# Performance work log

Hardware: AMD Instinct MI355X
Metric: run time of the kernel (lower is better)

Reference implementation:

```python
import jax, jax.numpy as jnp
import numpy as np

DIM = 1024
NUM_HEADS = 16
NUM_GROUPS = 4
HEAD_DIM = DIM // NUM_HEADS          # 64
HPG = NUM_HEADS // NUM_GROUPS        # heads per group = 4
SCALE = 1.0 / np.sqrt(HEAD_DIM)
LN_EPS = 1e-5


def layer_norm(x, w, b):
    # LayerNorm over last dim (head_dim), biased variance like torch.
    m = jnp.mean(x, axis=-1, keepdims=True)
    v = jnp.mean(jnp.square(x - m), axis=-1, keepdims=True)
    return (x - m) * jax.lax.rsqrt(v + LN_EPS) * w + b


def setup_inputs() -> dict:
    key = jax.random.key(0)
    ks = jax.random.split(key, 16)
    B, Q, KV = 2, 2048, 2048
    inv = 1.0 / np.sqrt(DIM)
    return {
        "query": jax.random.normal(ks[0], (B, Q, DIM), jnp.float32),
        "key": jax.random.normal(ks[1], (B, KV, DIM), jnp.float32),
        "value": jax.random.normal(ks[2], (B, KV, DIM), jnp.float32),
        "attn_mask": jnp.ones((B, Q, KV), dtype=bool),
        "Wq": jax.random.normal(ks[3], (DIM, DIM), jnp.float32) * inv,
        "bq": jnp.zeros((DIM,), jnp.float32),
        "Wk": jax.random.normal(ks[4], (NUM_GROUPS * HEAD_DIM, DIM), jnp.float32) * inv,
        "bk": jnp.zeros((NUM_GROUPS * HEAD_DIM,), jnp.float32),
        "Wv": jax.random.normal(ks[5], (NUM_GROUPS * HEAD_DIM, DIM), jnp.float32) * inv,
        "bv": jnp.zeros((NUM_GROUPS * HEAD_DIM,), jnp.float32),
        "q_norm_w": jnp.ones((HEAD_DIM,), jnp.float32),
        "q_norm_b": jnp.zeros((HEAD_DIM,), jnp.float32),
        "k_norm_w": jnp.ones((HEAD_DIM,), jnp.float32),
        "k_norm_b": jnp.zeros((HEAD_DIM,), jnp.float32),
        "Wo": jax.random.normal(ks[6], (DIM, DIM), jnp.float32) * inv,
        "bo": jnp.zeros((DIM,), jnp.float32),
    }


def reference(query, key, value, attn_mask, Wq, bq, Wk, bk, Wv, bv,
              q_norm_w, q_norm_b, k_norm_w, k_norm_b, Wo, bo):
    B, Q, _ = query.shape
    KV = key.shape[1]
    # projections (torch nn.Linear: x @ W.T + b)
    q = query @ Wq.T + bq                     # [B,Q,dim]
    k = key @ Wk.T + bk                       # [B,KV,G*hd]
    v = value @ Wv.T + bv                     # [B,KV,G*hd]
    # split heads: q -> [B, G, hpg, Q, hd]
    q = q.reshape(B, Q, NUM_GROUPS, HPG, HEAD_DIM).transpose(0, 2, 3, 1, 4)
    # k, v -> [B, G, KV, hd], broadcast over hpg
    k = k.reshape(B, KV, NUM_GROUPS, HEAD_DIM).transpose(0, 2, 1, 3)
    v = v.reshape(B, KV, NUM_GROUPS, HEAD_DIM).transpose(0, 2, 1, 3)
    # QK-norm per head_dim
    q = layer_norm(q, q_norm_w, q_norm_b)     # [B,G,hpg,Q,hd]
    k = layer_norm(k, k_norm_w, k_norm_b)     # [B,G,KV,hd]
    # attention scores: [B,G,hpg,Q,KV]
    scores = jnp.einsum('bghqd,bgkd->bghqk', q, k) * SCALE
    neg = jnp.asarray(jnp.finfo(scores.dtype).min, scores.dtype)
    scores = jnp.where(attn_mask[:, None, None, :, :], scores, neg)
    attn = jax.nn.softmax(scores, axis=-1)
    out = jnp.einsum('bghqk,bgkd->bghqd', attn, v)   # [B,G,hpg,Q,hd]
    out = out.transpose(0, 3, 1, 2, 4).reshape(B, Q, DIM)
    return out @ Wo.T + bo
```

## Files before the change

kernel.cpp:

```cpp
#include <hip/hip_runtime.h>
#include <math.h>

#define DIM   1024
#define NH    16
#define NG    4
#define HD    64
#define SEQ   2048
#define NB    2
#define SCALE 0.125f
#define LN_EPS 1e-5f
#define LOG2E 1.44269504f
#define QS    (SCALE * LOG2E)

#if __has_builtin(__builtin_amdgcn_exp2f)
#define EXP2F(x) __builtin_amdgcn_exp2f(x)
#else
#define EXP2F(x) __expf((x) * 0.69314718f)
#endif

typedef __attribute__((ext_vector_type(8)))  short short8;
typedef __attribute__((ext_vector_type(4)))  short short4v;
typedef __attribute__((ext_vector_type(4)))  float f32x4;
typedef __attribute__((ext_vector_type(16))) float f32x16;
typedef __attribute__((ext_vector_type(4)))  uint  uint4v;
typedef unsigned short ushort;
typedef unsigned int uint;

__device__ __forceinline__ ushort f2b(float f) {
  uint u = __builtin_bit_cast(uint, f);
  u += 0x7FFFu + ((u >> 16) & 1u);
  return (ushort)(u >> 16);
}
__device__ __forceinline__ uint pack2(float a, float b) {
  return (uint)f2b(a) | ((uint)f2b(b) << 16);
}
__device__ __forceinline__ uint packtr(float a, float b) {
  return __builtin_amdgcn_perm(__builtin_bit_cast(uint, b),
                               __builtin_bit_cast(uint, a), 0x07060302u);
}
__device__ __forceinline__ void gload16(const void* g, void* l) {
  __builtin_amdgcn_global_load_lds(
      (const __attribute__((address_space(1))) void*)g,
      (__attribute__((address_space(3))) void*)l, 16, 0, 0);
}

struct CastSeg { const float* s; ushort* d; int nblk; };
struct CastArgs { CastSeg seg[7]; };

__global__ __launch_bounds__(256) void castN(CastArgs a) {
  for (int t0 = blockIdx.x; t0 < 7424; t0 += gridDim.x) {
    int t = t0, i = 0;
    while (i < 6 && t >= a.seg[i].nblk) { t -= a.seg[i].nblk; ++i; }
    const float* src = a.seg[i].s;
    ushort* dst = a.seg[i].d;
    size_t idx = (size_t)t * 2048 + threadIdx.x * 8;
    float4 f0 = *(const float4*)(src + idx);
    float4 f1 = *(const float4*)(src + idx + 4);
    short8 o;
    o[0] = (short)f2b(f0.x); o[1] = (short)f2b(f0.y);
    o[2] = (short)f2b(f0.z); o[3] = (short)f2b(f0.w);
    o[4] = (short)f2b(f1.x); o[5] = (short)f2b(f1.y);
    o[6] = (short)f2b(f1.z); o[7] = (short)f2b(f1.w);
    *(short8*)(dst + idx) = o;
  }
}

#define STAGE2(dstLDS, srcG, NROWS, kk)                                        \
  _Pragma("unroll")                                                            \
  for (int i = 0; i < (NROWS) / 32; ++i) {                                     \
    int s = i * 256 + tid;                                                     \
    int row = s >> 3, cg = (s & 7) ^ (row & 7);                                \
    gload16(&(srcG)[(size_t)row * DIM + (kk) + cg * 8],                        \
            &(dstLDS)[(size_t)(i * 256 + (wave << 6)) * 8]);                   \
  }

#define CORE_128x64(Aptr, Wbase)                                               \
  f32x4 acc[2][4] = {};                                                        \
  { const int wm0 = wave * 32;                                                 \
    const ushort* Arows = (Aptr) + (size_t)m0 * DIM;                           \
    STAGE2(As[0], Arows, 128, 0)                                               \
    STAGE2(Ws[0], (Wbase), 64, 0)                                              \
    _Pragma("unroll")                                                          \
    for (int k0 = 0; k0 < DIM; k0 += 64) {                                     \
      const int pb = (k0 >> 6) & 1;                                            \
      __syncthreads();                                                         \
      if (k0 + 64 < DIM) {                                                     \
        STAGE2(As[1 - pb], Arows, 128, k0 + 64)                                \
        STAGE2(Ws[1 - pb], (Wbase), 64, k0 + 64)                               \
      }                                                                        \
      _Pragma("unroll")                                                        \
      for (int kh = 0; kh < 2; ++kh) {                                         \
        short8 af[2], bfr[4];                                                  \
        _Pragma("unroll")                                                      \
        for (int mt = 0; mt < 2; ++mt) {                                       \
          int row = wm0 + mt * 16 + l16;                                       \
          int st = (kh * 4 + quad) ^ (row & 7);                                \
          af[mt] = *(const short8*)&As[pb][row * 64 + st * 8];                 \
        }                                                                      \
        _Pragma("unroll")                                                      \
        for (int nt = 0; nt < 4; ++nt) {                                       \
          int row = nt * 16 + l16;                                             \
          int st = (kh * 4 + quad) ^ (row & 7);                                \
          bfr[nt] = *(const short8*)&Ws[pb][row * 64 + st * 8];                \
        }                                                                      \
        _Pragma("unroll")                                                      \
        for (int mt = 0; mt < 2; ++mt)                                         \
          _Pragma("unroll")                                                    \
          for (int nt = 0; nt < 4; ++nt)                                       \
            acc[mt][nt] = __builtin_amdgcn_mfma_f32_16x16x32_bf16(             \
                af[mt], bfr[nt], acc[mt][nt], 0, 0, 0);                        \
      }                                                                        \
    } }

#define LN_EPI(MT, rowbase, biasp, lnwp, lnbp, psv, outp, ostride, colb)       \
  { float bw[4], lw[4], lb[4];                                                 \
    _Pragma("unroll") for (int nt = 0; nt < 4; ++nt) {                         \
      bw[nt] = biasp[(colb) + nt * 16 + l16];                                  \
      lw[nt] = lnwp[nt * 16 + l16];                                            \
      lb[nt] = lnbp[nt * 16 + l16]; }                                          \
    _Pragma("unroll") for (int mt = 0; mt < (MT); ++mt) {                      \
      _Pragma("unroll") for (int r = 0; r < 4; ++r) {                          \
        float x0 = acc[mt][0][r] + bw[0];                                      \
        float x1 = acc[mt][1][r] + bw[1];                                      \
        float x2 = acc[mt][2][r] + bw[2];                                      \
        float x3 = acc[mt][3][r] + bw[3];                                      \
        float s1 = x0 + x1 + x2 + x3;                                          \
        float s2 = x0 * x0 + x1 * x1 + x2 * x2 + x3 * x3;                      \
        _Pragma("unroll") for (int off = 1; off < 16; off <<= 1) {             \
          s1 += __shfl_xor(s1, off, 64); s2 += __shfl_xor(s2, off, 64); }      \
        float mean = s1 * (1.f / 64.f);                                        \
        float var  = s2 * (1.f / 64.f) - mean * mean;                          \
        float inv  = rsqrtf(var + LN_EPS);                                     \
        int row = (rowbase) + mt * 16 + quad * 4 + r;                          \
        ushort* dst = outp + (size_t)row * (ostride) + (colb) + l16;           \
        dst[ 0] = f2b(((x0 - mean) * inv * lw[0] + lb[0]) * (psv));            \
        dst[16] = f2b(((x1 - mean) * inv * lw[1] + lb[1]) * (psv));            \
        dst[32] = f2b(((x2 - mean) * inv * lw[2] + lb[2]) * (psv));            \
        dst[48] = f2b(((x3 - mean) * inv * lw[3] + lb[3]) * (psv)); } } }

__global__ __launch_bounds__(256) void gemm_qkv(
    const ushort* __restrict__ qA, const ushort* __restrict__ kA,
    const ushort* __restrict__ vA,
    const ushort* __restrict__ WqB, const ushort* __restrict__ WkB,
    const ushort* __restrict__ WvB,
    const float* __restrict__ bq, const float* __restrict__ bk,
    const float* __restrict__ bv,
    const float* __restrict__ qnw, const float* __restrict__ qnb,
    const float* __restrict__ knw, const float* __restrict__ knb,
    ushort* __restrict__ Qb, ushort* __restrict__ kbb, ushort* __restrict__ vtb)
{
  __shared__ __align__(16) ushort As[2][128 * 64];
  __shared__ __align__(16) ushort Ws[2][64 * 64];
  const int bid = blockIdx.x;
  const int sw = (bid & 7) * 96 + (bid >> 3);
  const int x = sw % 24;
  const int tid = threadIdx.x;
  const int wave = tid >> 6, lane = tid & 63;
  const int quad = lane >> 4, l16 = lane & 15;
  const int m0 = (sw / 24) * 128;

  if (x < 16) {
    const ushort* Wbase = WqB + (size_t)x * 64 * DIM;
    CORE_128x64(qA, Wbase)
    LN_EPI(2, m0 + wave * 32, bq, qnw, qnb, QS, Qb, DIM, x * 64)
  } else if (x < 20) {
    const int n0 = (x - 16) * 64;
    const ushort* Wbase = WkB + (size_t)n0 * DIM;
    CORE_128x64(kA, Wbase)
    LN_EPI(2, m0 + wave * 32, bk, knw, knb, 1.0f, kbb, NG * HD, n0)
  } else {
    const int g = x - 20;
    const ushort* Wbase = WvB + (size_t)g * 64 * DIM;
    CORE_128x64(vA, Wbase)
#pragma unroll
    for (int nt = 0; nt < 4; ++nt) {
      int d = nt * 16 + l16;
      float bvv = bv[g * 64 + d];
#pragma unroll
      for (int mt = 0; mt < 2; ++mt)
#pragma unroll
        for (int r = 0; r < 4; ++r) {
          int row = m0 + wave * 32 + mt * 16 + quad * 4 + r;
          int bb = row >> 11, kv = row & (SEQ - 1);
          int kvp = (kv & ~12) | ((kv & 4) << 1) | ((kv & 8) >> 1);
          vtb[((size_t)(bb * NG + g) * HD + d) * SEQ + kvp] =
              f2b(acc[mt][nt][r] + bvv);
        }
    }
  }
}

__global__ __launch_bounds__(256) void gemm_out(
    const ushort* __restrict__ A, const ushort* __restrict__ WoB,
    const float* __restrict__ bo, float* __restrict__ Cf)
{
  __shared__ __align__(16) ushort As[2][128 * 64];
  __shared__ __align__(16) ushort Ws[2][64 * 64];
  const int bid = blockIdx.x;
  const int sw = (bid & 7) * 64 + (bid >> 3);
  const int tid = threadIdx.x;
  const int wave = tid >> 6, lane = tid & 63;
  const int quad = lane >> 4, l16 = lane & 15;
  const int m0 = (sw >> 4) * 128;
  const int n0 = (sw & 15) * 64;
  const ushort* Wbase = WoB + (size_t)n0 * DIM;
  CORE_128x64(A, Wbase)
#pragma unroll
  for (int nt = 0; nt < 4; ++nt) {
    int col = n0 + nt * 16 + l16;
    float bvv = bo[col];
#pragma unroll
    for (int mt = 0; mt < 2; ++mt)
#pragma unroll
      for (int r = 0; r < 4; ++r) {
        int row = m0 + wave * 32 + mt * 16 + quad * 4 + r;
        Cf[(size_t)row * DIM + col] = acc[mt][nt][r] + bvv;
      }
  }
}

__global__ __launch_bounds__(256) void attn_mfma4(
    const ushort* __restrict__ qb,
    const ushort* __restrict__ kb,
    const ushort* __restrict__ vt,
    ushort* __restrict__ op)
{
  __shared__ __align__(16) ushort SM[2][16384];
  const int bid = blockIdx.x;
  const int xcd = bid & 7, rest = bid >> 3;
  const int b = xcd >> 2, g = xcd & 3;
  const int h = g * 4 + (rest & 3);
  const int qt = rest >> 2;
  const int tid = threadIdx.x;
  const int wave = tid >> 6, lane = tid & 63;
  const int l32 = lane & 31, hf = lane >> 5;
  const int q0 = qt << 7;

  short8 qf[4];
  {
    const ushort* qp = qb + (size_t)(b * SEQ + q0 + wave * 32 + l32) * DIM
                          + h * HD + hf * 8;
#pragma unroll
    for (int ks = 0; ks < 4; ++ks) qf[ks] = *(const short8*)(qp + ks * 16);
  }

#define STAGE_ATTN(PB, KV0)                                                    \
  _Pragma("unroll")                                                            \
  for (int i = 0; i < 4; ++i) {                                                \
    int s = i * 256 + tid;                                                     \
    int rowK = s >> 3, cgK = (s & 7) ^ (rowK & 7);                             \
    gload16(&kb[(size_t)(b * SEQ + (KV0) + rowK) * (NG * HD) + g * HD + cgK * 8],\
            &SM[PB][(size_t)(i * 256 + (wave << 6)) * 8]);                     \
    int rowV = s >> 4, cgV = (s & 15) ^ (rowV & 7);                            \
    gload16(&vt[((size_t)(b * NG + g) * HD + rowV) * SEQ + (KV0) + cgV * 8],   \
            &SM[PB][8192 + (size_t)(i * 256 + (wave << 6)) * 8]);              \
  }

  f32x16 O0 = {0,0,0,0,0,0,0,0,0,0,0,0,0,0,0,0};
  f32x16 O1 = {0,0,0,0,0,0,0,0,0,0,0,0,0,0,0,0};
  float lsum = 0.f;

  STAGE_ATTN(0, 0)
  __syncthreads();

  for (int kv0 = 0; kv0 < SEQ; kv0 += 128) {
    const int pb = (kv0 >> 7) & 1;
    if (kv0 + 128 < SEQ) { STAGE_ATTN(1 - pb, kv0 + 128) }
    const ushort* Ks = SM[pb];
    const ushort* Vs = SM[pb] + 8192;

    f32x16 S0 = {0,0,0,0,0,0,0,0,0,0,0,0,0,0,0,0};
    f32x16 S1 = {0,0,0,0,0,0,0,0,0,0,0,0,0,0,0,0};
    f32x16 S2 = {0,0,0,0,0,0,0,0,0,0,0,0,0,0,0,0};
    f32x16 S3 = {0,0,0,0,0,0,0,0,0,0,0,0,0,0,0,0};
    __builtin_amdgcn_s_setprio(1);
#pragma unroll
    for (int ks = 0; ks < 4; ++ks) {
      short8 k0 = *(const short8*)&Ks[( 0 + l32) * 64 + (((ks*2+hf) ^ ( l32 & 7)) * 8)];
      short8 k1 = *(const short8*)&Ks[(32 + l32) * 64 + (((ks*2+hf) ^ ( l32 & 7)) * 8)];
      short8 k2 = *(const short8*)&Ks[(64 + l32) * 64 + (((ks*2+hf) ^ ( l32 & 7)) * 8)];
      short8 k3 = *(const short8*)&Ks[(96 + l32) * 64 + (((ks*2+hf) ^ ( l32 & 7)) * 8)];
      S0 = __builtin_amdgcn_mfma_f32_32x32x16_bf16(k0, qf[ks], S0, 0, 0, 0);
      S1 = __builtin_amdgcn_mfma_f32_32x32x16_bf16(k1, qf[ks], S1, 0, 0, 0);
      S2 = __builtin_amdgcn_mfma_f32_32x32x16_bf16(k2, qf[ks], S2, 0, 0, 0);
      S3 = __builtin_amdgcn_mfma_f32_32x32x16_bf16(k3, qf[ks], S3, 0, 0, 0);
    }
    __builtin_amdgcn_s_setprio(0);

#pragma unroll
    for (int t = 0; t < 8; ++t) {
      const f32x16& Ss = (t < 2) ? S0 : (t < 4) ? S1 : (t < 6) ? S2 : S3;
      int base = (t & 1) * 8;
      float e0 = EXP2F(Ss[base + 0]), e1 = EXP2F(Ss[base + 1]);
      float e2 = EXP2F(Ss[base + 2]), e3 = EXP2F(Ss[base + 3]);
      float e4 = EXP2F(Ss[base + 4]), e5 = EXP2F(Ss[base + 5]);
      float e6 = EXP2F(Ss[base + 6]), e7 = EXP2F(Ss[base + 7]);
      lsum += ((e0 + e1) + (e2 + e3)) + ((e4 + e5) + (e6 + e7));
      uint4v pw;
      pw[0] = packtr(e0, e1); pw[1] = packtr(e2, e3);
      pw[2] = packtr(e4, e5); pw[3] = packtr(e6, e7);
      short8 pf = __builtin_bit_cast(short8, pw);
      int ch = (t * 2 + hf);
      short8 v0 = *(const short8*)&Vs[( 0 + l32) * 128 + ((ch ^ ( l32 & 7)) * 8)];
      short8 v1 = *(const short8*)&Vs[(32 + l32) * 128 + ((ch ^ ( l32 & 7)) * 8)];
      __builtin_amdgcn_s_setprio(1);
      O0 = __builtin_amdgcn_mfma_f32_32x32x16_bf16(v0, pf, O0, 0, 0, 0);
      O1 = __builtin_amdgcn_mfma_f32_32x32x16_bf16(v1, pf, O1, 0, 0, 0);
      __builtin_amdgcn_s_setprio(0);
    }
    __syncthreads();
  }

  float inv = 1.f / (lsum + __shfl_xor(lsum, 32, 64));

  ushort* Lw = (ushort*)SM + wave * (32 * 68);
#pragma unroll
  for (int r = 0; r < 16; r += 2) {
    int d0 = (r & 3) + 8 * (r >> 2) + 4 * hf;
    *(uint*)&Lw[l32 * 68 + d0]      = pack2(O0[r] * inv, O0[r + 1] * inv);
    *(uint*)&Lw[l32 * 68 + 32 + d0] = pack2(O1[r] * inv, O1[r + 1] * inv);
  }
  ushort* orow = op + (size_t)(b * SEQ + q0 + wave * 32 + l32) * DIM
                    + h * HD + hf * 32;
#pragma unroll
  for (int c = 0; c < 4; ++c) {
    short4v lo = *(const short4v*)&Lw[l32 * 68 + hf * 32 + c * 8];
    short4v hi = *(const short4v*)&Lw[l32 * 68 + hf * 32 + c * 8 + 4];
    short8 o = {lo[0], lo[1], lo[2], lo[3], hi[0], hi[1], hi[2], hi[3]};
    *(short8*)(orow + c * 8) = o;
  }
#undef STAGE_ATTN
}

extern "C" void kernel_launch(void* const* d_in, const int* in_sizes, int n_in,
                              void* d_out, int out_size, void* d_ws, size_t ws_size,
                              hipStream_t stream) {
  (void)in_sizes; (void)n_in; (void)out_size; (void)ws_size;
  const float* query = (const float*)d_in[0];
  const float* key   = (const float*)d_in[1];
  const float* value = (const float*)d_in[2];
  const float* Wq = (const float*)d_in[4];
  const float* bq = (const float*)d_in[5];
  const float* Wk = (const float*)d_in[6];
  const float* bk = (const float*)d_in[7];
  const float* Wv = (const float*)d_in[8];
  const float* bv = (const float*)d_in[9];
  const float* qnw = (const float*)d_in[10];
  const float* qnb = (const float*)d_in[11];
  const float* knw = (const float*)d_in[12];
  const float* knb = (const float*)d_in[13];
  const float* Wo = (const float*)d_in[14];
  const float* bo = (const float*)d_in[15];
  float* out = (float*)d_out;

  const size_t MD = (size_t)NB * SEQ * DIM;
  const size_t WD = (size_t)DIM * DIM;
  const size_t KD = (size_t)(NG * HD) * DIM;
  const size_t MK = (size_t)NB * SEQ * NG * HD;

  ushort* qA  = (ushort*)d_ws;
  ushort* kA  = qA  + MD;
  ushort* WqB = kA  + MD;
  ushort* WkB = WqB + WD;
  ushort* WvB = WkB + KD;
  ushort* WoB = WvB + KD;
  ushort* Qb  = WoB + WD;
  ushort* vA  = (ushort*)d_out;
  ushort* kbb = vA  + MD;
  ushort* vtb = kbb + MK;
  ushort* attnO = kA;

  dim3 blk(256);
  CastArgs ca;
  ca.seg[0] = { query, qA, 2048 };
  ca.seg[1] = { key,   kA, 2048 };
  ca.seg[2] = { value, vA, 2048 };
  ca.seg[3] = { Wq, WqB, 512 };
  ca.seg[4] = { Wk, WkB, 128 };
  ca.seg[5] = { Wv, WvB, 128 };
  ca.seg[6] = { Wo, WoB, 512 };
  castN<<<dim3(1856), blk, 0, stream>>>(ca);
  gemm_qkv<<<dim3(768), blk, 0, stream>>>(
      qA, kA, vA, WqB, WkB, WvB, bq, bk, bv,
      qnw, qnb, knw, knb, Qb, kbb, vtb);
  attn_mfma4<<<dim3(512), blk, 0, stream>>>(Qb, kbb, vtb, attnO);
  gemm_out<<<dim3(512), blk, 0, stream>>>(attnO, WoB, bo, out);
}
```

Baseline: 223.7 us.

## Fuse cast into QKV GEMM and out-proj into attention via grid barriers

Merges the fp32-to-bf16 cast kernel into the QKV projection kernel, and the output projection into the attention kernel, with a software grid-wide atomic barrier between phases. This cuts launches from four to two (plus two small memsets) and removes inter-kernel gaps. The barriers rely on all 768 or 512 blocks being co-resident, which launch_bounds hints encourage but do not guarantee; otherwise the kernel deadlocks. Barrier counters are placed in scratch regions of d_out and the workspace that are reset by memset each call.

Measured after the change: 518.5 us. 132% more time.

```diff
diff --git a/kernel.cpp b/kernel.cpp
--- a/kernel.cpp
+++ b/kernel.cpp
@@ -44,26 +44,21 @@
       (__attribute__((address_space(3))) void*)l, 16, 0, 0);
 }
 
+__device__ __forceinline__ void grid_sync(uint* bar, uint nblk) {
+  __threadfence();
+  __syncthreads();
+  if (threadIdx.x == 0) {
+    __hip_atomic_fetch_add(bar, 1u, __ATOMIC_ACQ_REL, __HIP_MEMORY_SCOPE_AGENT);
+    while (__hip_atomic_load(bar, __ATOMIC_ACQUIRE, __HIP_MEMORY_SCOPE_AGENT)
+           < nblk)
+      __builtin_amdgcn_s_sleep(2);
+  }
+  __syncthreads();
+  __threadfence();
+}
+
 struct CastSeg { const float* s; ushort* d; int nblk; };
 struct CastArgs { CastSeg seg[7]; };
-
-__global__ __launch_bounds__(256) void castN(CastArgs a) {
-  for (int t0 = blockIdx.x; t0 < 7424; t0 += gridDim.x) {
-    int t = t0, i = 0;
-    while (i < 6 && t >= a.seg[i].nblk) { t -= a.seg[i].nblk; ++i; }
-    const float* src = a.seg[i].s;
-    ushort* dst = a.seg[i].d;
-    size_t idx = (size_t)t * 2048 + threadIdx.x * 8;
-    float4 f0 = *(const float4*)(src + idx);
-    float4 f1 = *(const float4*)(src + idx + 4);
-    short8 o;
-    o[0] = (short)f2b(f0.x); o[1] = (short)f2b(f0.y);
-    o[2] = (short)f2b(f0.z); o[3] = (short)f2b(f0.w);
-    o[4] = (short)f2b(f1.x); o[5] = (short)f2b(f1.y);
-    o[6] = (short)f2b(f1.z); o[7] = (short)f2b(f1.w);
-    *(short8*)(dst + idx) = o;
-  }
-}
 
 #define STAGE2(dstLDS, srcG, NROWS, kk)                                        \
   _Pragma("unroll")                                                            \
@@ -138,7 +133,8 @@
         dst[32] = f2b(((x2 - mean) * inv * lw[2] + lb[2]) * (psv));            \
         dst[48] = f2b(((x3 - mean) * inv * lw[3] + lb[3]) * (psv)); } } }
 
-__global__ __launch_bounds__(256) void gemm_qkv(
+__global__ __launch_bounds__(256, 3) void cast_qkv(
+    CastArgs ca,
     const ushort* __restrict__ qA, const ushort* __restrict__ kA,
     const ushort* __restrict__ vA,
     const ushort* __restrict__ WqB, const ushort* __restrict__ WkB,
@@ -147,14 +143,34 @@
     const float* __restrict__ bv,
     const float* __restrict__ qnw, const float* __restrict__ qnb,
     const float* __restrict__ knw, const float* __restrict__ knb,
-    ushort* __restrict__ Qb, ushort* __restrict__ kbb, ushort* __restrict__ vtb)
+    ushort* __restrict__ Qb, ushort* __restrict__ kbb, ushort* __restrict__ vtb,
+    uint* __restrict__ bar)
 {
   __shared__ __align__(16) ushort As[2][128 * 64];
   __shared__ __align__(16) ushort Ws[2][64 * 64];
+  const int tid = threadIdx.x;
+
+  for (int t0 = blockIdx.x; t0 < 7424; t0 += 768) {
+    int t = t0, i = 0;
+    while (i < 6 && t >= ca.seg[i].nblk) { t -= ca.seg[i].nblk; ++i; }
+    const float* src = ca.seg[i].s;
+    ushort* dst = ca.seg[i].d;
+    size_t idx = (size_t)t * 2048 + tid * 8;
+    float4 f0 = *(const float4*)(src + idx);
+    float4 f1 = *(const float4*)(src + idx + 4);
+    short8 o;
+    o[0] = (short)f2b(f0.x); o[1] = (short)f2b(f0.y);
+    o[2] = (short)f2b(f0.z); o[3] = (short)f2b(f0.w);
+    o[4] = (short)f2b(f1.x); o[5] = (short)f2b(f1.y);
+    o[6] = (short)f2b(f1.z); o[7] = (short)f2b(f1.w);
+    *(short8*)(dst + idx) = o;
+  }
+
+  grid_sync(bar, 768);
+
   const int bid = blockIdx.x;
   const int sw = (bid & 7) * 96 + (bid >> 3);
   const int x = sw % 24;
-  const int tid = threadIdx.x;
   const int wave = tid >> 6, lane = tid & 63;
   const int quad = lane >> 4, l16 = lane & 15;
   const int m0 = (sw / 24) * 128;
@@ -190,59 +206,35 @@
   }
 }
 
-__global__ __launch_bounds__(256) void gemm_out(
-    const ushort* __restrict__ A, const ushort* __restrict__ WoB,
-    const float* __restrict__ bo, float* __restrict__ Cf)
-{
-  __shared__ __align__(16) ushort As[2][128 * 64];
-  __shared__ __align__(16) ushort Ws[2][64 * 64];
-  const int bid = blockIdx.x;
-  const int sw = (bid & 7) * 64 + (bid >> 3);
-  const int tid = threadIdx.x;
-  const int wave = tid >> 6, lane = tid & 63;
-  const int quad = lane >> 4, l16 = lane & 15;
-  const int m0 = (sw >> 4) * 128;
-  const int n0 = (sw & 15) * 64;
-  const ushort* Wbase = WoB + (size_t)n0 * DIM;
-  CORE_128x64(A, Wbase)
-#pragma unroll
-  for (int nt = 0; nt < 4; ++nt) {
-    int col = n0 + nt * 16 + l16;
-    float bvv = bo[col];
-#pragma unroll
-    for (int mt = 0; mt < 2; ++mt)
-#pragma unroll
-      for (int r = 0; r < 4; ++r) {
-        int row = m0 + wave * 32 + mt * 16 + quad * 4 + r;
-        Cf[(size_t)row * DIM + col] = acc[mt][nt][r] + bvv;
-      }
-  }
-}
-
-__global__ __launch_bounds__(256) void attn_mfma4(
+__global__ __launch_bounds__(256, 2) void attn_out(
     const ushort* __restrict__ qb,
     const ushort* __restrict__ kb,
     const ushort* __restrict__ vt,
-    ushort* __restrict__ op)
+    ushort* __restrict__ op,
+    const ushort* __restrict__ WoB,
+    const float* __restrict__ bo, float* __restrict__ Cf,
+    uint* __restrict__ bar)
 {
   __shared__ __align__(16) ushort SM[2][16384];
   const int bid = blockIdx.x;
-  const int xcd = bid & 7, rest = bid >> 3;
-  const int b = xcd >> 2, g = xcd & 3;
-  const int h = g * 4 + (rest & 3);
-  const int qt = rest >> 2;
   const int tid = threadIdx.x;
   const int wave = tid >> 6, lane = tid & 63;
-  const int l32 = lane & 31, hf = lane >> 5;
-  const int q0 = qt << 7;
-
-  short8 qf[4];
+
   {
-    const ushort* qp = qb + (size_t)(b * SEQ + q0 + wave * 32 + l32) * DIM
-                          + h * HD + hf * 8;
-#pragma unroll
-    for (int ks = 0; ks < 4; ++ks) qf[ks] = *(const short8*)(qp + ks * 16);
-  }
+    const int xcd = bid & 7, rest = bid >> 3;
+    const int b = xcd >> 2, g = xcd & 3;
+    const int h = g * 4 + (rest & 3);
+    const int qt = rest >> 2;
+    const int l32 = lane & 31, hf = lane >> 5;
+    const int q0 = qt << 7;
+
+    short8 qf[4];
+    {
+      const ushort* qp = qb + (size_t)(b * SEQ + q0 + wave * 32 + l32) * DIM
+                            + h * HD + hf * 8;
+#pragma unroll
+      for (int ks = 0; ks < 4; ++ks) qf[ks] = *(const short8*)(qp + ks * 16);
+    }
 
 #define STAGE_ATTN(PB, KV0)                                                    \
   _Pragma("unroll")                                                            \
@@ -256,80 +248,108 @@
             &SM[PB][8192 + (size_t)(i * 256 + (wave << 6)) * 8]);              \
   }
 
-  f32x16 O0 = {0,0,0,0,0,0,0,0,0,0,0,0,0,0,0,0};
-  f32x16 O1 = {0,0,0,0,0,0,0,0,0,0,0,0,0,0,0,0};
-  float lsum = 0.f;
-
-  STAGE_ATTN(0, 0)
-  __syncthreads();
-
-  for (int kv0 = 0; kv0 < SEQ; kv0 += 128) {
-    const int pb = (kv0 >> 7) & 1;
-    if (kv0 + 128 < SEQ) { STAGE_ATTN(1 - pb, kv0 + 128) }
-    const ushort* Ks = SM[pb];
-    const ushort* Vs = SM[pb] + 8192;
-
-    f32x16 S0 = {0,0,0,0,0,0,0,0,0,0,0,0,0,0,0,0};
-    f32x16 S1 = {0,0,0,0,0,0,0,0,0,0,0,0,0,0,0,0};
-    f32x16 S2 = {0,0,0,0,0,0,0,0,0,0,0,0,0,0,0,0};
-    f32x16 S3 = {0,0,0,0,0,0,0,0,0,0,0,0,0,0,0,0};
-    __builtin_amdgcn_s_setprio(1);
-#pragma unroll
-    for (int ks = 0; ks < 4; ++ks) {
-      short8 k0 = *(const short8*)&Ks[( 0 + l32) * 64 + (((ks*2+hf) ^ ( l32 & 7)) * 8)];
-      short8 k1 = *(const short8*)&Ks[(32 + l32) * 64 + (((ks*2+hf) ^ ( l32 & 7)) * 8)];
-      short8 k2 = *(const short8*)&Ks[(64 + l32) * 64 + (((ks*2+hf) ^ ( l32 & 7)) * 8)];
-      short8 k3 = *(const short8*)&Ks[(96 + l32) * 64 + (((ks*2+hf) ^ ( l32 & 7)) * 8)];
-      S0 = __builtin_amdgcn_mfma_f32_32x32x16_bf16(k0, qf[ks], S0, 0, 0, 0);
-      S1 = __builtin_amdgcn_mfma_f32_32x32x16_bf16(k1, qf[ks], S1, 0, 0, 0);
-      S2 = __builtin_amdgcn_mfma_f32_32x32x16_bf16(k2, qf[ks], S2, 0, 0, 0);
-      S3 = __builtin_amdgcn_mfma_f32_32x32x16_bf16(k3, qf[ks], S3, 0, 0, 0);
-    }
-    __builtin_amdgcn_s_setprio(0);
-
-#pragma unroll
-    for (int t = 0; t < 8; ++t) {
-      const f32x16& Ss = (t < 2) ? S0 : (t < 4) ? S1 : (t < 6) ? S2 : S3;
-      int base = (t & 1) * 8;
-      float e0 = EXP2F(Ss[base + 0]), e1 = EXP2F(Ss[base + 1]);
-      float e2 = EXP2F(Ss[base + 2]), e3 = EXP2F(Ss[base + 3]);
-      float e4 = EXP2F(Ss[base + 4]), e5 = EXP2F(Ss[base + 5]);
-      float e6 = EXP2F(Ss[base + 6]), e7 = EXP2F(Ss[base + 7]);
-      lsum += ((e0 + e1) + (e2 + e3)) + ((e4 + e5) + (e6 + e7));
-      uint4v pw;
-      pw[0] = packtr(e0, e1); pw[1] = packtr(e2, e3);
-      pw[2] = packtr(e4, e5); pw[3] = packtr(e6, e7);
-      short8 pf = __builtin_bit_cast(short8, pw);
-      int ch = (t * 2 + hf);
-      short8 v0 = *(const short8*)&Vs[( 0 + l32) * 128 + ((ch ^ ( l32 & 7)) * 8)];
-      short8 v1 = *(const short8*)&Vs[(32 + l32) * 128 + ((ch ^ ( l32 & 7)) * 8)];
+    f32x16 O0 = {0,0,0,0,0,0,0,0,0,0,0,0,0,0,0,0};
+    f32x16 O1 = {0,0,0,0,0,0,0,0,0,0,0,0,0,0,0,0};
+    float lsum = 0.f;
+
+    STAGE_ATTN(0, 0)
+    __syncthreads();
+
+    for (int kv0 = 0; kv0 < SEQ; kv0 += 128) {
+      const int pb = (kv0 >> 7) & 1;
+      if (kv0 + 128 < SEQ) { STAGE_ATTN(1 - pb, kv0 + 128) }
+      const ushort* Ks = SM[pb];
+      const ushort* Vs = SM[pb] + 8192;
+
+      f32x16 S0 = {0,0,0,0,0,0,0,0,0,0,0,0,0,0,0,0};
+      f32x16 S1 = {0,0,0,0,0,0,0,0,0,0,0,0,0,0,0,0};
+      f32x16 S2 = {0,0,0,0,0,0,0,0,0,0,0,0,0,0,0,0};
+      f32x16 S3 = {0,0,0,0,0,0,0,0,0,0,0,0,0,0,0,0};
       __builtin_amdgcn_s_setprio(1);
-      O0 = __builtin_amdgcn_mfma_f32_32x32x16_bf16(v0, pf, O0, 0, 0, 0);
-      O1 = __builtin_amdgcn_mfma_f32_32x32x16_bf16(v1, pf, O1, 0, 0, 0);
+#pragma unroll
+      for (int ks = 0; ks < 4; ++ks) {
+        short8 k0 = *(const short8*)&Ks[( 0 + l32) * 64 + (((ks*2+hf) ^ ( l32 & 7)) * 8)];
+        short8 k1 = *(const short8*)&Ks[(32 + l32) * 64 + (((ks*2+hf) ^ ( l32 & 7)) * 8)];
+        short8 k2 = *(const short8*)&Ks[(64 + l32) * 64 + (((ks*2+hf) ^ ( l32 & 7)) * 8)];
+        short8 k3 = *(const short8*)&Ks[(96 + l32) * 64 + (((ks*2+hf) ^ ( l32 & 7)) * 8)];
+        S0 = __builtin_amdgcn_mfma_f32_32x32x16_bf16(k0, qf[ks], S0, 0, 0, 0);
+        S1 = __builtin_amdgcn_mfma_f32_32x32x16_bf16(k1, qf[ks], S1, 0, 0, 0);
+        S2 = __builtin_amdgcn_mfma_f32_32x32x16_bf16(k2, qf[ks], S2, 0, 0, 0);
+        S3 = __builtin_amdgcn_mfma_f32_32x32x16_bf16(k3, qf[ks], S3, 0, 0, 0);
+      }
       __builtin_amdgcn_s_setprio(0);
-    }
-    __syncthreads();
-  }
-
-  float inv = 1.f / (lsum + __shfl_xor(lsum, 32, 64));
-
-  ushort* Lw = (ushort*)SM + wave * (32 * 68);
-#pragma unroll
-  for (int r = 0; r < 16; r += 2) {
-    int d0 = (r & 3) + 8 * (r >> 2) + 4 * hf;
-    *(uint*)&Lw[l32 * 68 + d0]      = pack2(O0[r] * inv, O0[r + 1] * inv);
-    *(uint*)&Lw[l32 * 68 + 32 + d0] = pack2(O1[r] * inv, O1[r + 1] * inv);
-  }
-  ushort* orow = op + (size_t)(b * SEQ + q0 + wave * 32 + l32) * DIM
-                    + h * HD + hf * 32;
-#pragma unroll
-  for (int c = 0; c < 4; ++c) {
-    short4v lo = *(const short4v*)&Lw[l32 * 68 + hf * 32 + c * 8];
-    short4v hi = *(const short4v*)&Lw[l32 * 68 + hf * 32 + c * 8 + 4];
-    short8 o = {lo[0], lo[1], lo[2], lo[3], hi[0], hi[1], hi[2], hi[3]};
-    *(short8*)(orow + c * 8) = o;
-  }
+
+#pragma unroll
+      for (int t = 0; t < 8; ++t) {
+        const f32x16& Ss = (t < 2) ? S0 : (t < 4) ? S1 : (t < 6) ? S2 : S3;
+        int base = (t & 1) * 8;
+        float e0 = EXP2F(Ss[base + 0]), e1 = EXP2F(Ss[base + 1]);
+        float e2 = EXP2F(Ss[base + 2]), e3 = EXP2F(Ss[base + 3]);
+        float e4 = EXP2F(Ss[base + 4]), e5 = EXP2F(Ss[base + 5]);
+        float e6 = EXP2F(Ss[base + 6]), e7 = EXP2F(Ss[base + 7]);
+        lsum += ((e0 + e1) + (e2 + e3)) + ((e4 + e5) + (e6 + e7));
+        uint4v pw;
+        pw[0] = packtr(e0, e1); pw[1] = packtr(e2, e3);
+        pw[2] = packtr(e4, e5); pw[3] = packtr(e6, e7);
+        short8 pf = __builtin_bit_cast(short8, pw);
+        int ch = (t * 2 + hf);
+        short8 v0 = *(const short8*)&Vs[( 0 + l32) * 128 + ((ch ^ ( l32 & 7)) * 8)];
+        short8 v1 = *(const short8*)&Vs[(32 + l32) * 128 + ((ch ^ ( l32 & 7)) * 8)];
+        __builtin_amdgcn_s_setprio(1);
+        O0 = __builtin_amdgcn_mfma_f32_32x32x16_bf16(v0, pf, O0, 0, 0, 0);
+        O1 = __builtin_amdgcn_mfma_f32_32x32x16_bf16(v1, pf, O1, 0, 0, 0);
+        __builtin_amdgcn_s_setprio(0);
+      }
+      __syncthreads();
+    }
+
+    float inv = 1.f / (lsum + __shfl_xor(lsum, 32, 64));
+
+    const int l32e = lane & 31, hfe = lane >> 5;
+    ushort* Lw = (ushort*)SM + wave * (32 * 68);
+#pragma unroll
+    for (int r = 0; r < 16; r += 2) {
+      int d0 = (r & 3) + 8 * (r >> 2) + 4 * hfe;
+      *(uint*)&Lw[l32e * 68 + d0]      = pack2(O0[r] * inv, O0[r + 1] * inv);
+      *(uint*)&Lw[l32e * 68 + 32 + d0] = pack2(O1[r] * inv, O1[r + 1] * inv);
+    }
+    ushort* orow = op + (size_t)(b * SEQ + q0 + wave * 32 + l32e) * DIM
+                      + h * HD + hfe * 32;
+#pragma unroll
+    for (int c = 0; c < 4; ++c) {
+      short4v lo = *(const short4v*)&Lw[l32e * 68 + hfe * 32 + c * 8];
+      short4v hi = *(const short4v*)&Lw[l32e * 68 + hfe * 32 + c * 8 + 4];
+      short8 o = {lo[0], lo[1], lo[2], lo[3], hi[0], hi[1], hi[2], hi[3]};
+      *(short8*)(orow + c * 8) = o;
+    }
 #undef STAGE_ATTN
+  }
+
+  grid_sync(bar, 512);
+
+  {
+    ushort (*As)[128 * 64] = reinterpret_cast<ushort (*)[128 * 64]>(&SM[0][0]);
+    ushort (*Ws)[64 * 64] =
+        reinterpret_cast<ushort (*)[64 * 64]>((ushort*)SM + 16384);
+    const int quad = lane >> 4, l16 = lane & 15;
+    const int sw = (bid & 7) * 64 + (bid >> 3);
+    const int m0 = (sw >> 4) * 128;
+    const int n0 = (sw & 15) * 64;
+    const ushort* Wbase = WoB + (size_t)n0 * DIM;
+    CORE_128x64(op, Wbase)
+#pragma unroll
+    for (int nt = 0; nt < 4; ++nt) {
+      int col = n0 + nt * 16 + l16;
+      float bvv = bo[col];
+#pragma unroll
+      for (int mt = 0; mt < 2; ++mt)
+#pragma unroll
+        for (int r = 0; r < 4; ++r) {
+          int row = m0 + wave * 32 + mt * 16 + quad * 4 + r;
+          Cf[(size_t)row * DIM + col] = acc[mt][nt][r] + bvv;
+        }
+    }
+  }
 }
 
 extern "C" void kernel_launch(void* const* d_in, const int* in_sizes, int n_in,
@@ -370,6 +390,9 @@
   ushort* vtb = kbb + MK;
   ushort* attnO = kA;
 
+  uint* bar1 = (uint*)((char*)d_out + 15u * 1024 * 1024);
+  uint* bar2 = (uint*)qA;
+
   dim3 blk(256);
   CastArgs ca;
   ca.seg[0] = { query, qA, 2048 };
@@ -379,10 +402,12 @@
   ca.seg[4] = { Wk, WkB, 128 };
   ca.seg[5] = { Wv, WvB, 128 };
   ca.seg[6] = { Wo, WoB, 512 };
-  castN<<<dim3(1856), blk, 0, stream>>>(ca);
-  gemm_qkv<<<dim3(768), blk, 0, stream>>>(
-      qA, kA, vA, WqB, WkB, WvB, bq, bk, bv,
-      qnw, qnb, knw, knb, Qb, kbb, vtb);
-  attn_mfma4<<<dim3(512), blk, 0, stream>>>(Qb, kbb, vtb, attnO);
-  gemm_out<<<dim3(512), blk, 0, stream>>>(attnO, WoB, bo, out);
-}
+
+  hipMemsetAsync(bar1, 0, 4, stream);
+  cast_qkv<<<dim3(768), blk, 0, stream>>>(
+      ca, qA, kA, vA, WqB, WkB, WvB, bq, bk, bv,
+      qnw, qnb, knw, knb, Qb, kbb, vtb, bar1);
+  hipMemsetAsync(bar2, 0, 4, stream);
+  attn_out<<<dim3(512), blk, 0, stream>>>(
+      Qb, kbb, vtb, attnO, WoB, bo, out, bar2);
+}
```
